# Optimization experiments

Measured on AMD Instinct MI355X. Metric: run time of the kernel, lower is better.

The kernel has to match this reference:

```python
import jax, jax.numpy as jnp
import numpy as np

B, C, H, W, P = 4, 256, 128, 128, 2048
THR = 0.8
EPS = 1e-5  # torch BatchNorm default eps


def setup_inputs() -> dict:
    key = jax.random.key(0)
    ks = jax.random.split(key, 4)
    return {
        "x": jax.random.normal(ks[0], (B, C, H, W), jnp.float32),
        "edge": jax.random.uniform(ks[1], (B, 1, H, W), jnp.float32),
        "conv_adj_w": jax.random.normal(ks[2], (P, P), jnp.float32) * 0.02,
        "bn_adj_gamma": jnp.ones((P,), jnp.float32),
        "bn_adj_beta": jnp.zeros((P,), jnp.float32),
        "conv_wg_w": jax.random.normal(ks[3], (C, C), jnp.float32) * 0.05,
        "bn_wg_gamma": jnp.ones((C,), jnp.float32),
        "bn_wg_beta": jnp.zeros((C,), jnp.float32),
    }


def _bn_eval(z, gamma, beta, axis):
    # inference-mode BatchNorm1d with running_mean=0, running_var=1
    shape = [1] * z.ndim
    shape[axis] = -1
    inv = 1.0 / jnp.sqrt(jnp.asarray(1.0 + EPS, z.dtype))
    return z * inv * gamma.reshape(shape) + beta.reshape(shape)


def reference(x, edge, conv_adj_w, bn_adj_gamma, bn_adj_beta,
              conv_wg_w, bn_wg_gamma, bn_wg_beta):
    b, c, h, w = x.shape
    # edge[edge < thr] = 0, then topk over flattened H*W (get_upcog)
    e = jnp.where(edge < THR, jnp.zeros((), edge.dtype), edge).reshape(b, h * w)
    _, idx = jax.lax.top_k(e, P)                      # [B, P] int32

    # ps(): gather sampled features at topk locations -> [B, P, C]
    x_flat = x.reshape(b, c, h * w)                   # [B, C, HW]
    idx_e = jnp.broadcast_to(idx[:, None, :], (b, c, P))
    g = jnp.take_along_axis(x_flat, idx_e, axis=2).transpose(0, 2, 1)  # [B, P, C]

    # GCN: node-mixing 1x1 Conv1d + BN + ReLU + residual
    z = jnp.einsum('op,bpc->boc', conv_adj_w, g)      # [B, P, C]
    z = jax.nn.relu(_bn_eval(z, bn_adj_gamma, bn_adj_beta, axis=1)) + g
    # feature-mixing 1x1 Conv1d + BN + ReLU (on transposed [B, C, P])
    t = z.transpose(0, 2, 1)                          # [B, C, P]
    t = jnp.einsum('dc,bcp->bdp', conv_wg_w, t)       # [B, C, P]
    t = jax.nn.relu(_bn_eval(t, bn_wg_gamma, bn_wg_beta, axis=1))
    reasoned = t                                      # GCN transpose + ARE permute cancel -> [B, C, P]

    # scatter reasoned features back into x (topk indices are unique)
    out = jax.vmap(lambda xf, i, r: xf.at[:, i].set(r))(x_flat, idx, reasoned)
    return out.reshape(b, c, h, w)
```

## Files before the change

kernel.cpp:

```cpp
#include <hip/hip_runtime.h>
#include <stdint.h>

#define B_   4
#define C_   256
#define HW_  16384
#define P_   2048
#define THR_ 0.8f
#define INV_ 0.9999950000374997f

#define NCIDX(b) ((b) << 4)

#define OFF_NCAND 0
#define OFF_CAND  256
#define OFF_TOPK  524544
#define OFF_POS   557312
#define OFF_G     819456
#define OFF_GT    9208064
#define OFF_Z2    13402368
#define OFF_WADJB 17596672
#define OFF_WGB   25985280
#define OFF_R     OFF_G
#define OFF_RANK  OFF_Z2

typedef __attribute__((ext_vector_type(8))) short bf16x8;
typedef __attribute__((ext_vector_type(4))) float f32x4;

__device__ __forceinline__ ushort f2bf(float f) {
    union { float f; unsigned u; } a; a.f = f;
    unsigned r = (a.u + 0x7fffu + ((a.u >> 16) & 1u)) >> 16;
    return (ushort)r;
}
__device__ __forceinline__ float bf2f(ushort u) {
    union { unsigned u; float f; } a; a.u = (unsigned)u << 16;
    return a.f;
}

#define PREP_WADJ_BLOCKS 4096
#define PREP_WG_BLOCKS   64
#define PREP_ZERO_BLOCKS 128
#define PREP_GRID (PREP_WADJ_BLOCKS + PREP_WG_BLOCKS + PREP_ZERO_BLOCKS)

__global__ __launch_bounds__(256) void prep_kernel(const float* __restrict__ Wadj,
                                                   ushort* __restrict__ WadjB,
                                                   const float* __restrict__ Wg,
                                                   ushort* __restrict__ WgB,
                                                   int* __restrict__ pos,
                                                   int* __restrict__ rankbuf,
                                                   int* __restrict__ ncand) {
    int bid = blockIdx.x;
    if (bid < PREP_WADJ_BLOCKS) {
        int i = bid * 256 + threadIdx.x;
        float4 v = ((const float4*)Wadj)[i];
        ushort4 o; o.x = f2bf(v.x); o.y = f2bf(v.y); o.z = f2bf(v.z); o.w = f2bf(v.w);
        ((ushort4*)WadjB)[i] = o;
    } else if (bid < PREP_WADJ_BLOCKS + PREP_WG_BLOCKS) {
        int i = (bid - PREP_WADJ_BLOCKS) * 256 + threadIdx.x;
        float4 v = ((const float4*)Wg)[i];
        ushort4 o; o.x = f2bf(v.x); o.y = f2bf(v.y); o.z = f2bf(v.z); o.w = f2bf(v.w);
        ((ushort4*)WgB)[i] = o;
    } else {
        int zb = bid - PREP_WADJ_BLOCKS - PREP_WG_BLOCKS;
        int i = zb * 256 + threadIdx.x;
        int4 z = {0, 0, 0, 0};
        if (i < B_ * HW_ / 4) ((int4*)pos)[i] = z;
        else                  ((int4*)rankbuf)[i - B_ * HW_ / 4] = z;
        if (zb == 0 && threadIdx.x < 64) ncand[threadIdx.x] = 0;
    }
}

__global__ __launch_bounds__(256) void compact_kernel(const float* __restrict__ edge,
                                                      unsigned long long* __restrict__ cand,
                                                      int* __restrict__ ncand) {
    int b = blockIdx.x >> 6;
    int i = (blockIdx.x & 63) * 256 + threadIdx.x;
    float e = edge[b * HW_ + i];
    bool act = (e >= THR_);
    unsigned long long mask = __ballot(act);
    int lane = threadIdx.x & 63;
    int wid  = threadIdx.x >> 6;
    int before = __popcll(mask & ((1ull << lane) - 1ull));
    __shared__ int wcnt[4];
    __shared__ int base;
    if (lane == 0) wcnt[wid] = __popcll(mask);
    __syncthreads();
    if (threadIdx.x == 0) {
        int c0 = wcnt[0], c1 = wcnt[1], c2 = wcnt[2], c3 = wcnt[3];
        wcnt[0] = 0; wcnt[1] = c0; wcnt[2] = c0 + c1; wcnt[3] = c0 + c1 + c2;
        base = atomicAdd(&ncand[NCIDX(b)], c0 + c1 + c2 + c3);
    }
    __syncthreads();
    if (act) {
        int slot = base + wcnt[wid] + before;
        unsigned vb = __float_as_uint(e);
        cand[(size_t)b * HW_ + slot] =
            ((unsigned long long)vb << 32) | (unsigned long long)(0xFFFFFFFFu - (unsigned)i);
    }
}

__global__ __launch_bounds__(256) void rank_partial_kernel(
        const unsigned long long* __restrict__ cand,
        const int* __restrict__ ncand,
        int* __restrict__ rankbuf) {
    int b = blockIdx.z;
    int n = ncand[NCIDX(b)];
    int jb = blockIdx.x * 256, tb = blockIdx.y * 256;
    if (jb >= n || tb >= n) return;
    const unsigned long long* cb = cand + (size_t)b * HW_;
    __shared__ unsigned long long tile[256];
    int j = jb + threadIdx.x;
    unsigned long long kj = (j < n) ? cb[j] : 0ull;
    tile[threadIdx.x] = (tb + (int)threadIdx.x < n) ? cb[tb + threadIdx.x] : 0ull;
    __syncthreads();
    int cnt = 0;
#pragma unroll 16
    for (int k = 0; k < 256; ++k) cnt += (tile[k] > kj) ? 1 : 0;
    if (j < n && cnt) atomicAdd(&rankbuf[b * HW_ + j], cnt);
}

__global__ __launch_bounds__(256) void rank_finalize_kernel(
        const unsigned long long* __restrict__ cand,
        const int* __restrict__ ncand,
        const int* __restrict__ rankbuf,
        int* __restrict__ topk,
        int* __restrict__ pos,
        const float* __restrict__ edge) {
    int b = blockIdx.y;
    int n = ncand[NCIDX(b)];
    int j = blockIdx.x * 256 + threadIdx.x;
    if (j < n) {
        int rank = rankbuf[b * HW_ + j];
        if (rank < P_) {
            int idx = (int)(0xFFFFFFFFu - (unsigned)(cand[(size_t)b * HW_ + j] & 0xFFFFFFFFull));
            topk[b * P_ + rank] = idx;
            pos[b * HW_ + idx] = rank + 1;
        }
    }
    if (n < P_ && blockIdx.x == 0 && threadIdx.x == 0) {
        int cnt = n;
        for (int i = 0; i < HW_ && cnt < P_; ++i) {
            if (edge[b * HW_ + i] < THR_) {
                topk[b * P_ + cnt] = i;
                pos[b * HW_ + i] = cnt + 1;
                cnt++;
            }
        }
    }
}

__global__ __launch_bounds__(256) void gather_lds_kernel(const float* __restrict__ x,
                                                         const int* __restrict__ topk,
                                                         ushort* __restrict__ gT) {
    __shared__ float row[HW_];
    int bc = blockIdx.x;
    int b = bc >> 8;
    const float* xr = x + (size_t)bc * HW_;
#pragma unroll
    for (int i = 0; i < 16; ++i)
        ((float4*)row)[threadIdx.x + i * 256] = ((const float4*)xr)[threadIdx.x + i * 256];
    __syncthreads();
    const int* tk = topk + b * P_;
    int p0 = threadIdx.x * 8;
    int4 i0 = *(const int4*)&tk[p0];
    int4 i1 = *(const int4*)&tk[p0 + 4];
    ushort4 o0, o1;
    o0.x = f2bf(row[i0.x]); o0.y = f2bf(row[i0.y]); o0.z = f2bf(row[i0.z]); o0.w = f2bf(row[i0.w]);
    o1.x = f2bf(row[i1.x]); o1.y = f2bf(row[i1.y]); o1.z = f2bf(row[i1.z]); o1.w = f2bf(row[i1.w]);
    ushort* gp = gT + (size_t)bc * P_ + p0;
    *(ushort4*)gp = o0;
    *(ushort4*)(gp + 4) = o1;
}

#define MFMA16(AB, BB)                                                              \
    _Pragma("unroll")                                                               \
    for (int i = 0; i < 4; ++i)                                                     \
    _Pragma("unroll")                                                               \
        for (int j = 0; j < 4; ++j)                                                 \
            acc[i][j] = __builtin_amdgcn_mfma_f32_16x16x32_bf16(                    \
                __builtin_bit_cast(bf16x8, AB[i]),                                  \
                __builtin_bit_cast(bf16x8, BB[j]), acc[i][j], 0, 0, 0);

template<int MODE, int KDIM, int NTN, int WPB>
__global__ __launch_bounds__(64 * WPB) void gemm_wave_kernel(
        const ushort* __restrict__ A, const ushort* __restrict__ B,
        const float* __restrict__ gamma, const float* __restrict__ beta,
        const ushort* __restrict__ residT, void* __restrict__ out) {
    constexpr int KSTEPS = KDIM / 32;
    const int bid = blockIdx.x;
    const int wid = threadIdx.x >> 6;
    const int mt = (bid / NTN) * WPB + wid;
    const int nt = bid % NTN;
    const int lane = threadIdx.x & 63;
    const int quad = lane >> 4, ln = lane & 15;

    const ushort* pa[4];
    const ushort* pb[4];
#pragma unroll
    for (int i = 0; i < 4; ++i) {
        pa[i] = A + (size_t)(mt * 64 + i * 16 + ln) * KDIM + quad * 8;
        pb[i] = B + (size_t)(nt * 64 + i * 16 + ln) * KDIM + quad * 8;
    }

    f32x4 acc[4][4];
#pragma unroll
    for (int i = 0; i < 4; ++i)
#pragma unroll
        for (int j = 0; j < 4; ++j) acc[i][j] = (f32x4){0.f, 0.f, 0.f, 0.f};

    uint4 A4[4][4], B4[4][4];
#pragma unroll
    for (int t = 0; t < 4; ++t)
#pragma unroll
        for (int i = 0; i < 4; ++i) {
            A4[t][i] = *(const uint4*)(pa[i] + t * 32);
            B4[t][i] = *(const uint4*)(pb[i] + t * 32);
        }

    int koff = 4 * 32;
    for (int s = 0; s < KSTEPS - 4; s += 4) {
#pragma unroll
        for (int t = 0; t < 4; ++t) {
            MFMA16(A4[t], B4[t])
#pragma unroll
            for (int i = 0; i < 4; ++i) {
                A4[t][i] = *(const uint4*)(pa[i] + koff + t * 32);
                B4[t][i] = *(const uint4*)(pb[i] + koff + t * 32);
            }
        }
        koff += 128;
    }
#pragma unroll
    for (int t = 0; t < 4; ++t) {
        MFMA16(A4[t], B4[t])
    }

    float gm[16], bt[16];
#pragma unroll
    for (int i = 0; i < 4; ++i)
#pragma unroll
        for (int rg = 0; rg < 4; ++rg) {
            int row = mt * 64 + i * 16 + quad * 4 + rg;
            gm[i * 4 + rg] = gamma[row] * INV_;
            bt[i * 4 + rg] = beta[row];
        }

    if (MODE == 1) {
#pragma unroll
        for (int j = 0; j < 4; ++j) {
            int n = nt * 64 + j * 16 + ln;
            int bb = n >> 8;
            int cc = n & (C_ - 1);
            const ushort* gr = residT + (size_t)n * P_;
            ushort* op = (ushort*)out + (size_t)bb * P_ * C_ + cc;
#pragma unroll
            for (int i = 0; i < 4; ++i) {
                int rbase = mt * 64 + i * 16 + quad * 4;
                ushort4 rv = *(const ushort4*)&gr[rbase];
                float rf[4] = {bf2f(rv.x), bf2f(rv.y), bf2f(rv.z), bf2f(rv.w)};
#pragma unroll
                for (int rg = 0; rg < 4; ++rg) {
                    int row = rbase + rg;
                    float v = fmaxf(acc[i][j][rg] * gm[i * 4 + rg] + bt[i * 4 + rg], 0.f) + rf[rg];
                    op[(size_t)row * C_] = f2bf(v);
                }
            }
        }
    } else {
#pragma unroll
        for (int j = 0; j < 4; ++j) {
            int n = nt * 64 + j * 16 + ln;
            int bb = n >> 11;
            int pp = n & (P_ - 1);
            float* op = (float*)out + (size_t)bb * C_ * P_ + pp;
#pragma unroll
            for (int i = 0; i < 4; ++i)
#pragma unroll
                for (int rg = 0; rg < 4; ++rg) {
                    int row = mt * 64 + i * 16 + quad * 4 + rg;
                    op[(size_t)row * P_] =
                        fmaxf(acc[i][j][rg] * gm[i * 4 + rg] + bt[i * 4 + rg], 0.f);
                }
        }
    }
}

__global__ __launch_bounds__(256) void output_kernel(const float* __restrict__ x,
                                                     const int* __restrict__ pos,
                                                     const float* __restrict__ r,
                                                     float* __restrict__ out) {
    size_t v = (size_t)blockIdx.x * 256 + threadIdx.x;
    size_t e0 = v * 4;
    int hw = (int)(e0 & (HW_ - 1));
    int bc = (int)(e0 >> 14);
    int d = bc & (C_ - 1);
    int b = bc >> 8;
    float4 xv = *(const float4*)&x[e0];
    int4 pv = *(const int4*)&pos[b * HW_ + hw];
    const float* rrow = r + ((size_t)b * C_ + d) * P_;
    float4 ov = xv;
    if (pv.x) ov.x = rrow[pv.x - 1];
    if (pv.y) ov.y = rrow[pv.y - 1];
    if (pv.z) ov.z = rrow[pv.z - 1];
    if (pv.w) ov.w = rrow[pv.w - 1];
    *(float4*)&out[e0] = ov;
}

extern "C" void kernel_launch(void* const* d_in, const int* in_sizes, int n_in,
                              void* d_out, int out_size, void* d_ws, size_t ws_size,
                              hipStream_t stream) {
    const float* x    = (const float*)d_in[0];
    const float* edge = (const float*)d_in[1];
    const float* Wadj = (const float*)d_in[2];
    const float* ga   = (const float*)d_in[3];
    const float* be   = (const float*)d_in[4];
    const float* Wg   = (const float*)d_in[5];
    const float* gw   = (const float*)d_in[6];
    const float* bw   = (const float*)d_in[7];
    float* out = (float*)d_out;

    char* ws = (char*)d_ws;
    int*                ncand = (int*)(ws + OFF_NCAND);
    unsigned long long* cand  = (unsigned long long*)(ws + OFF_CAND);
    int*                topk  = (int*)(ws + OFF_TOPK);
    int*                pos   = (int*)(ws + OFF_POS);
    int*                rankb = (int*)(ws + OFF_RANK);
    ushort*             gT    = (ushort*)(ws + OFF_GT);
    ushort*             z2    = (ushort*)(ws + OFF_Z2);
    ushort*             WadjB = (ushort*)(ws + OFF_WADJB);
    ushort*             WgB   = (ushort*)(ws + OFF_WGB);
    float*              rbuf  = (float*)(ws + OFF_R);

    prep_kernel<<<PREP_GRID, 256, 0, stream>>>(Wadj, WadjB, Wg, WgB, pos, rankb, ncand);
    compact_kernel<<<B_ * 64, 256, 0, stream>>>(edge, cand, ncand);
    {
        dim3 grid(64, 64, B_);
        rank_partial_kernel<<<grid, 256, 0, stream>>>(cand, ncand, rankb);
    }
    {
        dim3 grid(64, B_);
        rank_finalize_kernel<<<grid, 256, 0, stream>>>(cand, ncand, rankb, topk, pos, edge);
    }
    gather_lds_kernel<<<B_ * C_, 256, 0, stream>>>(x, topk, gT);

    gemm_wave_kernel<1, 2048, 16, 2><<<256, 128, 0, stream>>>(WadjB, gT, ga, be, gT, z2);
    gemm_wave_kernel<2, 256, 128, 1><<<512, 64, 0, stream>>>(WgB, z2, gw, bw, nullptr, rbuf);

    output_kernel<<<(B_ * C_ * HW_) / 4 / 256, 256, 0, stream>>>(x, pos, rbuf, out);
}
```

Baseline: 221.5 us.

## Replace first GEMM with LDS double-buffered 128x128 block-tiled kernel

The node-mixing GEMM (2048x2048 weights times the gathered features) moves from a per-wave kernel that loads operands straight from global memory to a 256-thread kernel that stages 128x128 A and B tiles in shared memory with double buffering and register prefetch. Each operand tile is now shared by four waves, which cuts global and L2 traffic. The cost is a grid of only 128 blocks on a GPU with many CUs, plus one barrier per k-step. The rank_finalize launch size is rewritten as 64*4, which is the same value as before.

```diff
diff --git a/kernel.cpp b/kernel.cpp
--- a/kernel.cpp
+++ b/kernel.cpp
@@ -179,6 +179,105 @@
                 __builtin_bit_cast(bf16x8, AB[i]),                                  \
                 __builtin_bit_cast(bf16x8, BB[j]), acc[i][j], 0, 0, 0);
 
+#define G1_LDK 40
+__global__ __launch_bounds__(256) void gemm1_lds_kernel(
+        const ushort* __restrict__ A, const ushort* __restrict__ B,
+        const float* __restrict__ gamma, const float* __restrict__ beta,
+        const ushort* __restrict__ residT, ushort* __restrict__ out) {
+    __shared__ ushort Asm[2][128][G1_LDK];
+    __shared__ ushort Bsm[2][128][G1_LDK];
+    const int mtb = blockIdx.x >> 3;
+    const int ntb = blockIdx.x & 7;
+    const int w   = threadIdx.x >> 6;
+    const int wr  = w >> 1, wc = w & 1;
+    const int lane = threadIdx.x & 63;
+    const int quad = lane >> 4, ln = lane & 15;
+    const int srow = lane >> 2;
+    const int sslot = lane & 3;
+
+    const ushort* gpa = A + (size_t)(mtb * 128 + w * 32 + srow) * 2048 + sslot * 8;
+    const ushort* gpb = B + (size_t)(ntb * 128 + w * 32 + srow) * 2048 + sslot * 8;
+
+    f32x4 acc[4][4];
+#pragma unroll
+    for (int i = 0; i < 4; ++i)
+#pragma unroll
+        for (int j = 0; j < 4; ++j) acc[i][j] = (f32x4){0.f, 0.f, 0.f, 0.f};
+
+    uint4 ga[2], gb[2];
+#pragma unroll
+    for (int m = 0; m < 2; ++m) {
+        ga[m] = *(const uint4*)(gpa + (size_t)m * 16 * 2048);
+        gb[m] = *(const uint4*)(gpb + (size_t)m * 16 * 2048);
+    }
+#pragma unroll
+    for (int m = 0; m < 2; ++m) {
+        *(uint4*)&Asm[0][w * 32 + m * 16 + srow][sslot * 8] = ga[m];
+        *(uint4*)&Bsm[0][w * 32 + m * 16 + srow][sslot * 8] = gb[m];
+    }
+    __syncthreads();
+
+    for (int t = 0; t < 64; ++t) {
+        const int cur = t & 1;
+        if (t < 63) {
+            const int ko = (t + 1) * 32;
+#pragma unroll
+            for (int m = 0; m < 2; ++m) {
+                ga[m] = *(const uint4*)(gpa + (size_t)m * 16 * 2048 + ko);
+                gb[m] = *(const uint4*)(gpb + (size_t)m * 16 * 2048 + ko);
+            }
+        }
+        {
+            uint4 av[4], bv[4];
+#pragma unroll
+            for (int i = 0; i < 4; ++i) {
+                av[i] = *(const uint4*)&Asm[cur][wr * 64 + i * 16 + ln][quad * 8];
+                bv[i] = *(const uint4*)&Bsm[cur][wc * 64 + i * 16 + ln][quad * 8];
+            }
+            MFMA16(av, bv)
+        }
+        if (t < 63) {
+#pragma unroll
+            for (int m = 0; m < 2; ++m) {
+                *(uint4*)&Asm[cur ^ 1][w * 32 + m * 16 + srow][sslot * 8] = ga[m];
+                *(uint4*)&Bsm[cur ^ 1][w * 32 + m * 16 + srow][sslot * 8] = gb[m];
+            }
+        }
+        __syncthreads();
+    }
+
+    const int mte = mtb * 2 + wr;
+    const int nte = ntb * 2 + wc;
+    float gm[16], bt[16];
+#pragma unroll
+    for (int i = 0; i < 4; ++i)
+#pragma unroll
+        for (int rg = 0; rg < 4; ++rg) {
+            int row = mte * 64 + i * 16 + quad * 4 + rg;
+            gm[i * 4 + rg] = gamma[row] * INV_;
+            bt[i * 4 + rg] = beta[row];
+        }
+#pragma unroll
+    for (int j = 0; j < 4; ++j) {
+        int n = nte * 64 + j * 16 + ln;
+        int bb = n >> 8;
+        int cc = n & (C_ - 1);
+        const ushort* gr = residT + (size_t)n * P_;
+        ushort* op = out + (size_t)bb * P_ * C_ + cc;
+#pragma unroll
+        for (int i = 0; i < 4; ++i) {
+            int rbase = mte * 64 + i * 16 + quad * 4;
+            ushort4 rv = *(const ushort4*)&gr[rbase];
+            float rf[4] = {bf2f(rv.x), bf2f(rv.y), bf2f(rv.z), bf2f(rv.w)};
+#pragma unroll
+            for (int rg = 0; rg < 4; ++rg) {
+                float v = fmaxf(acc[i][j][rg] * gm[i * 4 + rg] + bt[i * 4 + rg], 0.f) + rf[rg];
+                op[(size_t)(rbase + rg) * C_] = f2bf(v);
+            }
+        }
+    }
+}
+
 template<int MODE, int KDIM, int NTN, int WPB>
 __global__ __launch_bounds__(64 * WPB) void gemm_wave_kernel(
         const ushort* __restrict__ A, const ushort* __restrict__ B,
@@ -337,11 +436,11 @@
     }
     {
         dim3 grid(64, B_);
-        rank_finalize_kernel<<<grid, 256, 0, stream>>>(cand, ncand, rankb, topk, pos, edge);
+        rank_finalize_kernel<<<grid, 64 * 4, 0, stream>>>(cand, ncand, rankb, topk, pos, edge);
     }
     gather_lds_kernel<<<B_ * C_, 256, 0, stream>>>(x, topk, gT);
 
-    gemm_wave_kernel<1, 2048, 16, 2><<<256, 128, 0, stream>>>(WadjB, gT, ga, be, gT, z2);
+    gemm1_lds_kernel<<<128, 256, 0, stream>>>(WadjB, gT, ga, be, gT, z2);
     gemm_wave_kernel<2, 256, 128, 1><<<512, 64, 0, stream>>>(WgB, z2, gw, bw, nullptr, rbuf);
 
     output_kernel<<<(B_ * C_ * HW_) / 4 / 256, 256, 0, stream>>>(x, pos, rbuf, out);
```

After: 226.1 us. 1.02x slower.
